# Optimization experiments

Measured on AMD Instinct MI355X. Metric: run time of the kernel, lower is better.

The kernel has to match this reference:

```python
import jax, jax.numpy as jnp
import numpy as np

N, M, FEAT, POS, D, MSG, NCLS = 64, 32, 256, 6, 262, 128, 7


def setup_inputs() -> dict:
    key = jax.random.key(0)
    ks = jax.random.split(key, 12)
    s = 0.05
    p = lambda k, shape: jax.random.normal(k, shape, jnp.float32) * s
    return {
        "nodes_feature": jax.random.normal(ks[0], (N, M, FEAT), jnp.float32),
        "pos": jax.random.normal(ks[1], (N, M, POS), jnp.float32),
        "num_rec": jax.random.randint(ks[2], (N,), 1, M + 1),
        "link_w1": p(ks[3], (D, 2 * D)),
        "link_b1": jnp.zeros((D,), jnp.float32),
        "link_w2": p(ks[4], (D,)),
        "link_b2": jnp.zeros((), jnp.float32),
        "msg_w": p(ks[5], (MSG, D)),
        "msg_b": jnp.zeros((MSG,), jnp.float32),
        "gru_w_ih": p(ks[6], (3 * D, MSG)),
        "gru_w_hh": p(ks[7], (3 * D, D)),
        "gru_b_ih": jnp.zeros((3 * D,), jnp.float32),
        "gru_b_hh": jnp.zeros((3 * D,), jnp.float32),
        "ro_w1": p(ks[8], (MSG, D)),
        "ro_b1": jnp.zeros((MSG,), jnp.float32),
        "ro_w2": p(ks[9], (NCLS, MSG)),
        "ro_b2": jnp.zeros((NCLS,), jnp.float32),
    }


def reference(nodes_feature, pos, num_rec, link_w1, link_b1, link_w2, link_b2,
              msg_w, msg_b, gru_w_ih, gru_w_hh, gru_b_ih, gru_b_hh,
              ro_w1, ro_b1, ro_w2, ro_b2):
    # node_feat = [resnet_feat, pos]  -> (N, M, 262)
    nf = jnp.concatenate([nodes_feature, pos], axis=-1)
    n, m, d = nf.shape
    valid = jnp.arange(m)[None, :] < num_rec[:, None]          # (N, M)
    pair = valid[:, :, None] & valid[:, None, :]               # (N, M, M)

    # edge_feat[b,:,i,j] = concat(nf[b,i], nf[b,j]); zero for invalid pairs
    ef = jnp.concatenate([
        jnp.broadcast_to(nf[:, :, None, :], (n, m, m, d)),
        jnp.broadcast_to(nf[:, None, :, :], (n, m, m, d)),
    ], axis=-1) * pair[..., None].astype(nf.dtype)             # (N, M, M, 2D)

    # 1x1 convs == per-pair MLP
    hlink = jax.nn.relu(jnp.einsum('bnwc,dc->bnwd', ef, link_w1) + link_b1)
    attmat = jax.nn.sigmoid(jnp.einsum('bnwd,d->bnw', hlink, link_w2) + link_b2)

    # messages are only summed over valid sender nodes w
    att_m = attmat * valid[:, None, :].astype(attmat.dtype)    # (N, M, M)

    def gru_step(x, h):
        # PyTorch GRU cell: gates order (r, z, n)
        gx = x @ gru_w_ih.T + gru_b_ih
        gh = h @ gru_w_hh.T + gru_b_hh
        xr, xz, xn = jnp.split(gx, 3, axis=-1)
        hr, hz, hn = jnp.split(gh, 3, axis=-1)
        r = jax.nn.sigmoid(xr + hr)
        z = jax.nn.sigmoid(xz + hz)
        c = jnp.tanh(xn + r * hn)
        return (1.0 - z) * c + z * h

    vmask = valid[..., None].astype(nf.dtype)
    h_state = nf                                               # pass 0 input state
    for _ in range(2):                                         # two message-passing rounds
        msg = h_state @ msg_w.T + msg_b                        # (N, M, 128)
        m_v = jnp.einsum('bnw,bwk->bnk', att_m, msg)           # attention-weighted sum
        h_state = gru_step(m_v, h_state) * vmask               # invalid nodes stay zero

    pred = (jax.nn.relu(h_state @ ro_w1.T + ro_b1) @ ro_w2.T + ro_b2) * vmask
    return pred, attmat
```

## Files before the change

### kernel.cpp

```cpp
#include <hip/hip_runtime.h>
#include <math.h>

#define N_G   64
#define M_N   32
#define FEAT  256
#define POSD  6
#define D     262
#define MSG   128
#define NCLS  7

#define KHW   288
#define KFULL 416
#define HSTR  416
#define PSTR  320

#define S_PROJ (528*288)
#define S_MSG  (128*288)
#define S_RZ   (544*416)
#define S_XN   (272*128)
#define S_HN   (272*288)
#define S_RO   (128*288)
#define S_RO2  (16*128)

#define O_WPROJ 0u
#define O_WMSG  76032u
#define O_WRZ   94464u
#define O_WXN   207616u
#define O_WHN   225024u
#define O_WRO   264192u
#define O_WRO2  282624u
#define O_GB    283648u
#define O_GHA   284736u
#define O_GHB   710720u
#define O_GPA   1136704u
#define O_GPB   1464384u
#define O_GATT  1792064u
#define O_GMSG  1833024u
#define O_B1P   1996864u
#define O_W2P   1997184u

typedef __attribute__((ext_vector_type(8))) short short8;
typedef __attribute__((ext_vector_type(4))) short short4v;
typedef __attribute__((ext_vector_type(4))) float floatx4;

#define MFMA __builtin_amdgcn_mfma_f32_16x16x32_bf16

__device__ __forceinline__ short f2bf(float f) {
    union { float f; unsigned u; } v; v.f = f;
    unsigned r = v.u + 0x7FFF + ((v.u >> 16) & 1);
    return (short)(r >> 16);
}
__device__ __forceinline__ float bf2f(short s) {
    union { float f; unsigned u; } v;
    v.u = ((unsigned)(unsigned short)s) << 16;
    return v.f;
}
__device__ __forceinline__ float sigf(float x) {
    return __builtin_amdgcn_rcpf(1.f + __expf(-x));
}
__device__ __forceinline__ float tanh_fast(float x) {
    float e = __expf(-2.f * fabsf(x));
    float t = (1.f - e) * __builtin_amdgcn_rcpf(1.f + e);
    return copysignf(t, x);
}

__global__ __launch_bounds__(256) void prep_kernel(
    const float* __restrict__ w1, const float* __restrict__ msg_w,
    const float* __restrict__ w_ih, const float* __restrict__ w_hh,
    const float* __restrict__ ro_w1, const float* __restrict__ ro_w2,
    const float* __restrict__ b_ih, const float* __restrict__ b_hh,
    const float* __restrict__ b1g, const float* __restrict__ w2g,
    const float* __restrict__ nodes, const float* __restrict__ pos,
    float* __restrict__ ws)
{
    short* wproj = (short*)(ws + O_WPROJ);
    short* wmsg  = (short*)(ws + O_WMSG);
    short* wrz   = (short*)(ws + O_WRZ);
    short* wxn   = (short*)(ws + O_WXN);
    short* whn   = (short*)(ws + O_WHN);
    short* wro   = (short*)(ws + O_WRO);
    short* wro2  = (short*)(ws + O_WRO2);
    float* gb    = ws + O_GB;

    int row = blockIdx.x * 4 + (threadIdx.x >> 6);
    const int lane = threadIdx.x & 63;
    if (row >= 5989) return;

    if (row < 528) {
        const int n = row;
        short* out = wproj + n * 288;
        const float* src = (n < D) ? (w1 + n * 524) : (w1 + (n - D) * 524 + D);
        for (int k = lane; k < 288; k += 64)
            out[k] = f2bf((k < D && n < 524) ? src[k] : 0.f);
        return;
    }
    row -= 528;
    if (row < 128) {
        short* out = wmsg + row * 288;
        const float* src = msg_w + row * D;
        for (int k = lane; k < 288; k += 64)
            out[k] = f2bf(k < D ? src[k] : 0.f);
        return;
    }
    row -= 128;
    if (row < 544) {
        const int g = row;
        const int gi = (g < 272) ? 0 : 1;
        const int d = g - gi * 272;
        short* out = wrz + g * 416;
        if (d < D) {
            const int r = gi * D + d;
            const float* sih = w_ih + r * MSG;
            const float* shh = w_hh + r * D - 128;
            for (int k = lane; k < 416; k += 64) {
                float v;
                if (k < 128)            v = sih[k];
                else if (k < 128 + D)   v = shh[k];
                else                    v = 0.f;
                out[k] = f2bf(v);
            }
        } else {
            for (int k = lane; k < 416; k += 64) out[k] = 0;
        }
        return;
    }
    row -= 544;
    if (row < 272) {
        const int d = row;
        short* out = wxn + d * 128;
        const float* src = w_ih + (2 * D + d) * MSG;
        for (int k = lane; k < 128; k += 64)
            out[k] = f2bf(d < D ? src[k] : 0.f);
        return;
    }
    row -= 272;
    if (row < 272) {
        const int d = row;
        short* out = whn + d * 288;
        const float* src = w_hh + (2 * D + d) * D;
        for (int k = lane; k < 288; k += 64)
            out[k] = f2bf((d < D && k < D) ? src[k] : 0.f);
        return;
    }
    row -= 272;
    if (row < 128) {
        short* out = wro + row * 288;
        const float* src = ro_w1 + row * D;
        for (int k = lane; k < 288; k += 64)
            out[k] = f2bf(k < D ? src[k] : 0.f);
        return;
    }
    row -= 128;
    if (row < 16) {
        short* out = wro2 + row * 128;
        const float* src = ro_w2 + row * MSG;
        for (int k = lane; k < 128; k += 64)
            out[k] = f2bf(row < NCLS ? src[k] : 0.f);
        return;
    }
    row -= 16;
    if (row < 4) {
        const int seg = row;
        float* out = gb + seg * 272;
        for (int d = lane; d < 272; d += 64) {
            float v = 0.f;
            if (d < D) {
                if (seg == 0)      v = b_ih[d] + b_hh[d];
                else if (seg == 1) v = b_ih[D + d] + b_hh[D + d];
                else if (seg == 2) v = b_ih[2 * D + d];
                else               v = b_hh[2 * D + d];
            }
            out[d] = v;
        }
        return;
    }
    row -= 4;
    if (row < 1) {
        float* b1p = ws + O_B1P;
        float* w2p = ws + O_W2P;
        for (int k = lane; k < 320; k += 64) {
            b1p[k] = (k < D) ? b1g[k] : 0.f;
            w2p[k] = (k < D) ? w2g[k] : 0.f;
        }
        return;
    }
    row -= 1;
    if (row < 2048) {
        const int b = row >> 5, w = row & 31;
        short* out = (short*)(ws + O_GHA) + (size_t)(b * 32 + w) * HSTR + 128;
        const float* nsrc = nodes + (size_t)(b * 32 + w) * FEAT;
        const float* psrc = pos + (size_t)(b * 32 + w) * POSD;
        for (int k = lane; k < 288; k += 64) {
            float v = 0.f;
            if (k < FEAT)             v = nsrc[k];
            else if (k < FEAT + POSD) v = psrc[k - FEAT];
            out[k] = f2bf(v);
        }
        return;
    }
    row -= 2048;
    {
        const int b = row >> 5, w = row & 31;
        short* hb = (short*)(ws + O_GHB) + (size_t)(b * 32 + w) * HSTR + 128;
        short* pa = (short*)(ws + O_GPA) + (size_t)(b * 32 + w) * PSTR;
        short* pb = (short*)(ws + O_GPB) + (size_t)(b * 32 + w) * PSTR;
        if (lane < 26) hb[D + lane] = 0;
        if (lane < 58) { pa[D + lane] = 0; pb[D + lane] = 0; }
    }
}

__global__ __launch_bounds__(256, 2) void k_proj(
    const float* __restrict__ ws, const float* __restrict__ msg_bg)
{
    const short* GH   = (const short*)(ws + O_GHA);
    short* GPA        = (short*)(ws + O_GPA);
    short* GPB        = (short*)(ws + O_GPB);
    short* GMSG       = (short*)(ws + O_GMSG);
    const short* Wproj = (const short*)(ws + O_WPROJ);
    const short* Wmsg  = (const short*)(ws + O_WMSG);

    const int job = blockIdx.x * 4 + (threadIdx.x >> 6);
    const int b = job / 41, t = job % 41;
    const int lane = threadIdx.x & 63;
    const int quad = lane >> 4, lrow = lane & 15;

    const short* ap0 = GH + (size_t)(b * 32 + lrow) * HSTR + 128 + quad * 8;
    const short* ap1 = ap0 + 16 * HSTR;
    const short* bw = (t < 33)
        ? Wproj + (t * 16 + lrow) * KHW + quad * 8
        : Wmsg + ((t - 33) * 16 + lrow) * KHW + quad * 8;

    short8 a0[9], a1[9], wv[9];
#pragma unroll
    for (int kk = 0; kk < 9; ++kk) {
        a0[kk] = *(const short8*)(ap0 + kk * 32);
        a1[kk] = *(const short8*)(ap1 + kk * 32);
        wv[kk] = *(const short8*)(bw + kk * 32);
    }
    floatx4 acc0 = {}, acc1 = {};
#pragma unroll
    for (int kk = 0; kk < 9; ++kk) {
        acc0 = MFMA(a0[kk], wv[kk], acc0, 0, 0, 0);
        acc1 = MFMA(a1[kk], wv[kk], acc1, 0, 0, 0);
    }
    if (t < 33) {
        int col = t * 16 + lrow;
#pragma unroll
        for (int rr = 0; rr < 4; ++rr) {
            int r0 = quad * 4 + rr;
            if (col < D) {
                GPA[(size_t)(b * 32 + r0) * PSTR + col] = f2bf(acc0[rr]);
                GPA[(size_t)(b * 32 + r0 + 16) * PSTR + col] = f2bf(acc1[rr]);
            } else if (col < 2 * D) {
                GPB[(size_t)(b * 32 + r0) * PSTR + (col - D)] = f2bf(acc0[rr]);
                GPB[(size_t)(b * 32 + r0 + 16) * PSTR + (col - D)] = f2bf(acc1[rr]);
            }
        }
    } else {
        int col = (t - 33) * 16 + lrow;
        float bias = msg_bg[col];
#pragma unroll
        for (int rr = 0; rr < 4; ++rr) {
            GMSG[(size_t)b * 5120 + col * 40 + quad * 4 + rr] = f2bf(acc0[rr] + bias);
            GMSG[(size_t)b * 5120 + col * 40 + 16 + quad * 4 + rr] = f2bf(acc1[rr] + bias);
        }
    }
}

__global__ __launch_bounds__(256, 4) void k_att(
    const float* __restrict__ ws, const int* __restrict__ nrec_g,
    const float* __restrict__ b2g, float* __restrict__ att_out)
{
    const short* GPA = (const short*)(ws + O_GPA);
    const short* GPB = (const short*)(ws + O_GPB);
    short* GATT      = (short*)(ws + O_GATT);
    const float* b1p = ws + O_B1P;
    const float* w2p = ws + O_W2P;

    const int g = blockIdx.x * 16 + (threadIdx.x >> 4);
    const int b = g >> 6;
    const int rem = g & 63;
    const int i = rem >> 1, jh = (rem & 1) * 16;
    const int c16 = threadIdx.x & 15;
    const int nr = nrec_g[b];
    const float b2v = b2g[0];

    float pav[5][4], b1v[5][4], w2v[5][4];
#pragma unroll
    for (int k = 0; k < 5; ++k) {
        int dbase = c16 * 4 + 64 * k;
        short4v p = *(const short4v*)(GPA + (size_t)(b * 32 + i) * PSTR + dbase);
        floatx4 bb = *(const floatx4*)(b1p + dbase);
        floatx4 ww = *(const floatx4*)(w2p + dbase);
#pragma unroll
        for (int e = 0; e < 4; ++e) {
            pav[k][e] = bf2f(p[e]); b1v[k][e] = bb[e]; w2v[k][e] = ww[e];
        }
    }
    float p0 = 0.f;
#pragma unroll
    for (int k = 0; k < 5; ++k)
#pragma unroll
        for (int e = 0; e < 4; ++e)
            p0 += fmaxf(b1v[k][e], 0.f) * w2v[k][e];
    p0 += __shfl_down(p0, 8, 16); p0 += __shfl_down(p0, 4, 16);
    p0 += __shfl_down(p0, 2, 16); p0 += __shfl_down(p0, 1, 16);
    float c0 = sigf(p0 + b2v);
    const bool vi = i < nr;
    for (int jj = 0; jj < 16; ++jj) {
        int j = jh + jj;
        float a;
        if (j < nr && vi) {
            const short* pb = GPB + (size_t)(b * 32 + j) * PSTR + c16 * 4;
            float s = 0.f;
#pragma unroll
            for (int k = 0; k < 5; ++k) {
                short4v q = *(const short4v*)(pb + 64 * k);
#pragma unroll
                for (int e = 0; e < 4; ++e) {
                    float v = pav[k][e] + bf2f(q[e]) + b1v[k][e];
                    s += fmaxf(v, 0.f) * w2v[k][e];
                }
            }
            s += __shfl_down(s, 8, 16); s += __shfl_down(s, 4, 16);
            s += __shfl_down(s, 2, 16); s += __shfl_down(s, 1, 16);
            a = sigf(s + b2v);
        } else {
            a = c0;
        }
        if (c16 == 0) {
            att_out[((size_t)(b * 32 + i)) * 32 + j] = a;
            GATT[(size_t)b * 1280 + i * 40 + j] = f2bf((j < nr) ? a : 0.f);
        }
    }
}

__global__ __launch_bounds__(256, 4) void k_mix0(float* __restrict__ ws)
{
    const short* GATT = (const short*)(ws + O_GATT);
    const short* GMSG = (const short*)(ws + O_GMSG);
    short* GH         = (short*)(ws + O_GHA);

    const int b = blockIdx.x;
    const int tid = threadIdx.x;
    const int ng = tid >> 6, lane = tid & 63;
    const int quad = lane >> 4, lrow = lane & 15;

    short8 af0 = *(const short8*)(GATT + (size_t)b * 1280 + lrow * 40 + quad * 8);
    short8 af1 = *(const short8*)(GATT + (size_t)b * 1280 + (16 + lrow) * 40 + quad * 8);
    short8 bf0 = *(const short8*)(GMSG + (size_t)b * 5120 + (ng * 32 + lrow) * 40 + quad * 8);
    short8 bf1 = *(const short8*)(GMSG + (size_t)b * 5120 + (ng * 32 + 16 + lrow) * 40 + quad * 8);
    floatx4 c00 = {}, c01 = {}, c10 = {}, c11 = {};
    c00 = MFMA(af0, bf0, c00, 0, 0, 0);
    c01 = MFMA(af0, bf1, c01, 0, 0, 0);
    c10 = MFMA(af1, bf0, c10, 0, 0, 0);
    c11 = MFMA(af1, bf1, c11, 0, 0, 0);
#pragma unroll
    for (int rr = 0; rr < 4; ++rr) {
        int m0 = quad * 4 + rr;
        GH[(size_t)(b * 32 + m0) * HSTR + ng * 32 + lrow] = f2bf(c00[rr]);
        GH[(size_t)(b * 32 + m0) * HSTR + ng * 32 + 16 + lrow] = f2bf(c01[rr]);
        GH[(size_t)(b * 32 + m0 + 16) * HSTR + ng * 32 + lrow] = f2bf(c10[rr]);
        GH[(size_t)(b * 32 + m0 + 16) * HSTR + ng * 32 + 16 + lrow] = f2bf(c11[rr]);
    }
}

__global__ __launch_bounds__(256, 2) void k_gru(
    float* __restrict__ ws, const int* __restrict__ nrec_g, const int srcA)
{
    const short* src = (const short*)(ws + (srcA ? O_GHA : O_GHB));
    short* dst       = (short*)(ws + (srcA ? O_GHB : O_GHA));
    const short* Wrz = (const short*)(ws + O_WRZ);
    const short* Wxn = (const short*)(ws + O_WXN);
    const short* Whn = (const short*)(ws + O_WHN);
    const float* gb  = ws + O_GB;

    const int job = blockIdx.x * 4 + (threadIdx.x >> 6);
    const int b = job / 17, s = job % 17;
    const int nr = nrec_g[b];
    const int lane = threadIdx.x & 63;
    const int quad = lane >> 4, lrow = lane & 15;

    const short* ap0 = src + (size_t)(b * 32 + lrow) * HSTR + quad * 8;
    const short* ap1 = ap0 + 16 * HSTR;
    short8 aA0[13], aA1[13];
#pragma unroll
    for (int kk = 0; kk < 13; ++kk) {
        aA0[kk] = *(const short8*)(ap0 + kk * 32);
        aA1[kk] = *(const short8*)(ap1 + kk * 32);
    }
    const short* bpr = Wrz + (s * 16 + lrow) * KFULL + quad * 8;
    const short* bpz = bpr + 272 * KFULL;
    const short* bpx = Wxn + (s * 16 + lrow) * 128 + quad * 8;
    const short* bph = Whn + (s * 16 + lrow) * KHW + quad * 8;

    short8 wr[13];
#pragma unroll
    for (int kk = 0; kk < 13; ++kk) wr[kk] = *(const short8*)(bpr + kk * 32);

    floatx4 aR0 = {}, aR1 = {}, aZ0 = {}, aZ1 = {};
    floatx4 aN0 = {}, aN1 = {}, aH0 = {}, aH1 = {};
#pragma unroll
    for (int kk = 0; kk < 13; ++kk) {
        aR0 = MFMA(aA0[kk], wr[kk], aR0, 0, 0, 0);
        aR1 = MFMA(aA1[kk], wr[kk], aR1, 0, 0, 0);
        if (kk < 4) {
            short8 bx = *(const short8*)(bpx + kk * 32);
            aN0 = MFMA(aA0[kk], bx, aN0, 0, 0, 0);
            aN1 = MFMA(aA1[kk], bx, aN1, 0, 0, 0);
        }
        wr[kk] = *(const short8*)(bpz + kk * 32);
    }
#pragma unroll
    for (int kk = 0; kk < 13; ++kk) {
        aZ0 = MFMA(aA0[kk], wr[kk], aZ0, 0, 0, 0);
        aZ1 = MFMA(aA1[kk], wr[kk], aZ1, 0, 0, 0);
        if (kk < 9) wr[kk] = *(const short8*)(bph + kk * 32);
    }
#pragma unroll
    for (int kk = 0; kk < 9; ++kk) {
        aH0 = MFMA(aA0[kk + 4], wr[kk], aH0, 0, 0, 0);
        aH1 = MFMA(aA1[kk + 4], wr[kk], aH1, 0, 0, 0);
    }

    const int d = s * 16 + lrow;
    if (d < D) {
        float bgr = gb[d], bgz = gb[272 + d];
        float bxv = gb[544 + d], bhv = gb[816 + d];
#pragma unroll
        for (int i = 0; i < 2; ++i) {
            floatx4 vR = i ? aR1 : aR0, vZ = i ? aZ1 : aZ0;
            floatx4 vN = i ? aN1 : aN0, vH = i ? aH1 : aH0;
#pragma unroll
            for (int rr = 0; rr < 4; ++rr) {
                int m = i * 16 + quad * 4 + rr;
                float rg = sigf(vR[rr] + bgr);
                float zg = sigf(vZ[rr] + bgz);
                float cg = tanh_fast(vN[rr] + bxv + rg * (vH[rr] + bhv));
                float hold = bf2f(src[(size_t)(b * 32 + m) * HSTR + 128 + d]);
                float hv = (1.f - zg) * cg + zg * hold;
                if (m >= nr) hv = 0.f;
                dst[(size_t)(b * 32 + m) * HSTR + 128 + d] = f2bf(hv);
            }
        }
    }
}

__global__ __launch_bounds__(256, 2) void k_msgmix1(
    float* __restrict__ ws, const float* __restrict__ msg_bg)
{
    __shared__ __align__(16) short msgT[128 * 40];
    short* GHB        = (short*)(ws + O_GHB);
    const short* GATT = (const short*)(ws + O_GATT);
    const short* Wmsg = (const short*)(ws + O_WMSG);

    const int b = blockIdx.x;
    const int tid = threadIdx.x;
    const int wave = tid >> 6, lane = tid & 63;
    const int quad = lane >> 4, lrow = lane & 15;

    const short* ap0 = GHB + (size_t)(b * 32 + lrow) * HSTR + 128 + quad * 8;
    const short* ap1 = ap0 + 16 * HSTR;
    short8 a0[9], a1[9];
#pragma unroll
    for (int kk = 0; kk < 9; ++kk) {
        a0[kk] = *(const short8*)(ap0 + kk * 32);
        a1[kk] = *(const short8*)(ap1 + kk * 32);
    }
#pragma unroll
    for (int ti = 0; ti < 2; ++ti) {
        int s = wave + ti * 4;
        const short* bw = Wmsg + (s * 16 + lrow) * KHW + quad * 8;
        short8 wv[9];
#pragma unroll
        for (int kk = 0; kk < 9; ++kk) wv[kk] = *(const short8*)(bw + kk * 32);
        floatx4 acc0 = {}, acc1 = {};
#pragma unroll
        for (int kk = 0; kk < 9; ++kk) {
            acc0 = MFMA(a0[kk], wv[kk], acc0, 0, 0, 0);
            acc1 = MFMA(a1[kk], wv[kk], acc1, 0, 0, 0);
        }
        int col = s * 16 + lrow;
        float bias = msg_bg[col];
#pragma unroll
        for (int rr = 0; rr < 4; ++rr) {
            msgT[col * 40 + quad * 4 + rr] = f2bf(acc0[rr] + bias);
            msgT[col * 40 + 16 + quad * 4 + rr] = f2bf(acc1[rr] + bias);
        }
    }
    __syncthreads();
    {
        const int ng = wave;
        short8 af0 = *(const short8*)(GATT + (size_t)b * 1280 + lrow * 40 + quad * 8);
        short8 af1 = *(const short8*)(GATT + (size_t)b * 1280 + (16 + lrow) * 40 + quad * 8);
        short8 bf0 = *(const short8*)(msgT + (ng * 32 + lrow) * 40 + quad * 8);
        short8 bf1 = *(const short8*)(msgT + (ng * 32 + 16 + lrow) * 40 + quad * 8);
        floatx4 c00 = {}, c01 = {}, c10 = {}, c11 = {};
        c00 = MFMA(af0, bf0, c00, 0, 0, 0);
        c01 = MFMA(af0, bf1, c01, 0, 0, 0);
        c10 = MFMA(af1, bf0, c10, 0, 0, 0);
        c11 = MFMA(af1, bf1, c11, 0, 0, 0);
#pragma unroll
        for (int rr = 0; rr < 4; ++rr) {
            int m0 = quad * 4 + rr;
            GHB[(size_t)(b * 32 + m0) * HSTR + ng * 32 + lrow] = f2bf(c00[rr]);
            GHB[(size_t)(b * 32 + m0) * HSTR + ng * 32 + 16 + lrow] = f2bf(c01[rr]);
            GHB[(size_t)(b * 32 + m0 + 16) * HSTR + ng * 32 + lrow] = f2bf(c10[rr]);
            GHB[(size_t)(b * 32 + m0 + 16) * HSTR + ng * 32 + 16 + lrow] = f2bf(c11[rr]);
        }
    }
}

__global__ __launch_bounds__(256, 2) void k_out(
    const float* __restrict__ ws, const int* __restrict__ nrec_g,
    const float* __restrict__ ro_b1g, const float* __restrict__ ro_b2g,
    float* __restrict__ pred)
{
    __shared__ __align__(16) short hidL[32 * 136];
    const short* GHA  = (const short*)(ws + O_GHA);
    const short* Wro  = (const short*)(ws + O_WRO);
    const short* Wro2 = (const short*)(ws + O_WRO2);

    const int b = blockIdx.x;
    const int tid = threadIdx.x;
    const int wave = tid >> 6, lane = tid & 63;
    const int quad = lane >> 4, lrow = lane & 15;
    const int nr = nrec_g[b];

    const short* ap0 = GHA + (size_t)(b * 32 + lrow) * HSTR + 128 + quad * 8;
    const short* ap1 = ap0 + 16 * HSTR;
    short8 a0[9], a1[9];
#pragma unroll
    for (int kk = 0; kk < 9; ++kk) {
        a0[kk] = *(const short8*)(ap0 + kk * 32);
        a1[kk] = *(const short8*)(ap1 + kk * 32);
    }
#pragma unroll
    for (int ti = 0; ti < 2; ++ti) {
        int s = wave + ti * 4;
        const short* bw = Wro + (s * 16 + lrow) * KHW + quad * 8;
        short8 wv[9];
#pragma unroll
        for (int kk = 0; kk < 9; ++kk) wv[kk] = *(const short8*)(bw + kk * 32);
        floatx4 acc0 = {}, acc1 = {};
#pragma unroll
        for (int kk = 0; kk < 9; ++kk) {
            acc0 = MFMA(a0[kk], wv[kk], acc0, 0, 0, 0);
            acc1 = MFMA(a1[kk], wv[kk], acc1, 0, 0, 0);
        }
        int col = s * 16 + lrow;
        float bias = ro_b1g[col];
#pragma unroll
        for (int rr = 0; rr < 4; ++rr) {
            hidL[(quad * 4 + rr) * 136 + col] = f2bf(fmaxf(acc0[rr] + bias, 0.f));
            hidL[(16 + quad * 4 + rr) * 136 + col] = f2bf(fmaxf(acc1[rr] + bias, 0.f));
        }
    }
    __syncthreads();
    if (wave == 0) {
        const short* bw = Wro2 + lrow * 128 + quad * 8;
        short8 wv[4];
#pragma unroll
        for (int kk = 0; kk < 4; ++kk) wv[kk] = *(const short8*)(bw + kk * 32);
        floatx4 acc0 = {}, acc1 = {};
        const short* ap = hidL + lrow * 136 + quad * 8;
#pragma unroll
        for (int kk = 0; kk < 4; ++kk) {
            short8 x0 = *(const short8*)(ap + kk * 32);
            short8 x1 = *(const short8*)(ap + 16 * 136 + kk * 32);
            acc0 = MFMA(x0, wv[kk], acc0, 0, 0, 0);
            acc1 = MFMA(x1, wv[kk], acc1, 0, 0, 0);
        }
        int q = lrow;
        if (q < NCLS) {
            float bias = ro_b2g[q];
#pragma unroll
            for (int i = 0; i < 2; ++i) {
#pragma unroll
                for (int rr = 0; rr < 4; ++rr) {
                    int m = i * 16 + quad * 4 + rr;
                    float v = (i ? acc1[rr] : acc0[rr]) + bias;
                    if (m >= nr) v = 0.f;
                    pred[((size_t)(b * 32 + m)) * NCLS + q] = v;
                }
            }
        }
    }
}

extern "C" void kernel_launch(void* const* d_in, const int* in_sizes, int n_in,
                              void* d_out, int out_size, void* d_ws, size_t ws_size,
                              hipStream_t stream)
{
    const float* nodes = (const float*)d_in[0];
    const float* pos   = (const float*)d_in[1];
    const int*   nrec  = (const int*)d_in[2];
    const float* w1    = (const float*)d_in[3];
    const float* b1    = (const float*)d_in[4];
    const float* w2    = (const float*)d_in[5];
    const float* b2    = (const float*)d_in[6];
    const float* msg_w = (const float*)d_in[7];
    const float* msg_b = (const float*)d_in[8];
    const float* w_ih  = (const float*)d_in[9];
    const float* w_hh  = (const float*)d_in[10];
    const float* b_ih  = (const float*)d_in[11];
    const float* b_hh  = (const float*)d_in[12];
    const float* ro_w1 = (const float*)d_in[13];
    const float* ro_b1 = (const float*)d_in[14];
    const float* ro_w2 = (const float*)d_in[15];
    const float* ro_b2 = (const float*)d_in[16];
    float* ws   = (float*)d_ws;
    float* pred = (float*)d_out;
    float* attout = pred + (size_t)N_G * M_N * NCLS;

    prep_kernel<<<1498, 256, 0, stream>>>(w1, msg_w, w_ih, w_hh, ro_w1, ro_w2,
                                          b_ih, b_hh, b1, w2, nodes, pos, ws);
    k_proj<<<656, 256, 0, stream>>>(ws, msg_b);
    k_att<<<256, 256, 0, stream>>>(ws, nrec, b2, attout);
    k_mix0<<<64, 256, 0, stream>>>(ws);
    k_gru<<<272, 256, 0, stream>>>(ws, nrec, 1);
    k_msgmix1<<<64, 256, 0, stream>>>(ws, msg_b);
    k_gru<<<272, 256, 0, stream>>>(ws, nrec, 0);
    k_out<<<64, 256, 0, stream>>>(ws, nrec, ro_b1, ro_b2, pred);
}
```

Baseline: 150.7 us.

## Fuse mix, GRU rounds, message and readout into one per-graph tail kernel

Replaces the five tail kernels (mix0, two GRU passes, msgmix1, readout) with a single 512-thread kernel per graph that keeps the hidden state double-buffered in shared memory across both message-passing rounds. It also prefetches the GRU weights into registers/cache at kernel start and drops the now-unneeded GHB/pad zeroing from prep. This removes several launches and global round trips of the hidden state. In exchange, only 64 blocks run the GRU, where previously it was spread over 272 blocks, so parallelism across CUs drops sharply.

```diff
diff --git a/kernel.cpp b/kernel.cpp
--- a/kernel.cpp
+++ b/kernel.cpp
@@ -9,18 +9,11 @@
 #define MSG   128
 #define NCLS  7
 
+#define KA_S  424
 #define KHW   288
 #define KFULL 416
 #define HSTR  416
 #define PSTR  320
-
-#define S_PROJ (528*288)
-#define S_MSG  (128*288)
-#define S_RZ   (544*416)
-#define S_XN   (272*128)
-#define S_HN   (272*288)
-#define S_RO   (128*288)
-#define S_RO2  (16*128)
 
 #define O_WPROJ 0u
 #define O_WMSG  76032u
@@ -31,7 +24,6 @@
 #define O_WRO2  282624u
 #define O_GB    283648u
 #define O_GHA   284736u
-#define O_GHB   710720u
 #define O_GPA   1136704u
 #define O_GPB   1464384u
 #define O_GATT  1792064u
@@ -73,22 +65,13 @@
     const float* __restrict__ nodes, const float* __restrict__ pos,
     float* __restrict__ ws)
 {
-    short* wproj = (short*)(ws + O_WPROJ);
-    short* wmsg  = (short*)(ws + O_WMSG);
-    short* wrz   = (short*)(ws + O_WRZ);
-    short* wxn   = (short*)(ws + O_WXN);
-    short* whn   = (short*)(ws + O_WHN);
-    short* wro   = (short*)(ws + O_WRO);
-    short* wro2  = (short*)(ws + O_WRO2);
-    float* gb    = ws + O_GB;
-
     int row = blockIdx.x * 4 + (threadIdx.x >> 6);
     const int lane = threadIdx.x & 63;
-    if (row >= 5989) return;
+    if (row >= 3941) return;
 
     if (row < 528) {
         const int n = row;
-        short* out = wproj + n * 288;
+        short* out = (short*)(ws + O_WPROJ) + n * 288;
         const float* src = (n < D) ? (w1 + n * 524) : (w1 + (n - D) * 524 + D);
         for (int k = lane; k < 288; k += 64)
             out[k] = f2bf((k < D && n < 524) ? src[k] : 0.f);
@@ -96,7 +79,7 @@
     }
     row -= 528;
     if (row < 128) {
-        short* out = wmsg + row * 288;
+        short* out = (short*)(ws + O_WMSG) + row * 288;
         const float* src = msg_w + row * D;
         for (int k = lane; k < 288; k += 64)
             out[k] = f2bf(k < D ? src[k] : 0.f);
@@ -107,7 +90,7 @@
         const int g = row;
         const int gi = (g < 272) ? 0 : 1;
         const int d = g - gi * 272;
-        short* out = wrz + g * 416;
+        short* out = (short*)(ws + O_WRZ) + g * 416;
         if (d < D) {
             const int r = gi * D + d;
             const float* sih = w_ih + r * MSG;
@@ -127,7 +110,7 @@
     row -= 544;
     if (row < 272) {
         const int d = row;
-        short* out = wxn + d * 128;
+        short* out = (short*)(ws + O_WXN) + d * 128;
         const float* src = w_ih + (2 * D + d) * MSG;
         for (int k = lane; k < 128; k += 64)
             out[k] = f2bf(d < D ? src[k] : 0.f);
@@ -136,7 +119,7 @@
     row -= 272;
     if (row < 272) {
         const int d = row;
-        short* out = whn + d * 288;
+        short* out = (short*)(ws + O_WHN) + d * 288;
         const float* src = w_hh + (2 * D + d) * D;
         for (int k = lane; k < 288; k += 64)
             out[k] = f2bf((d < D && k < D) ? src[k] : 0.f);
@@ -144,7 +127,7 @@
     }
     row -= 272;
     if (row < 128) {
-        short* out = wro + row * 288;
+        short* out = (short*)(ws + O_WRO) + row * 288;
         const float* src = ro_w1 + row * D;
         for (int k = lane; k < 288; k += 64)
             out[k] = f2bf(k < D ? src[k] : 0.f);
@@ -152,7 +135,7 @@
     }
     row -= 128;
     if (row < 16) {
-        short* out = wro2 + row * 128;
+        short* out = (short*)(ws + O_WRO2) + row * 128;
         const float* src = ro_w2 + row * MSG;
         for (int k = lane; k < 128; k += 64)
             out[k] = f2bf(row < NCLS ? src[k] : 0.f);
@@ -161,7 +144,7 @@
     row -= 16;
     if (row < 4) {
         const int seg = row;
-        float* out = gb + seg * 272;
+        float* out = ws + O_GB + seg * 272;
         for (int d = lane; d < 272; d += 64) {
             float v = 0.f;
             if (d < D) {
@@ -185,7 +168,7 @@
         return;
     }
     row -= 1;
-    if (row < 2048) {
+    {
         const int b = row >> 5, w = row & 31;
         short* out = (short*)(ws + O_GHA) + (size_t)(b * 32 + w) * HSTR + 128;
         const float* nsrc = nodes + (size_t)(b * 32 + w) * FEAT;
@@ -196,26 +179,16 @@
             else if (k < FEAT + POSD) v = psrc[k - FEAT];
             out[k] = f2bf(v);
         }
-        return;
-    }
-    row -= 2048;
-    {
-        const int b = row >> 5, w = row & 31;
-        short* hb = (short*)(ws + O_GHB) + (size_t)(b * 32 + w) * HSTR + 128;
-        short* pa = (short*)(ws + O_GPA) + (size_t)(b * 32 + w) * PSTR;
-        short* pb = (short*)(ws + O_GPB) + (size_t)(b * 32 + w) * PSTR;
-        if (lane < 26) hb[D + lane] = 0;
-        if (lane < 58) { pa[D + lane] = 0; pb[D + lane] = 0; }
     }
 }
 
 __global__ __launch_bounds__(256, 2) void k_proj(
     const float* __restrict__ ws, const float* __restrict__ msg_bg)
 {
-    const short* GH   = (const short*)(ws + O_GHA);
-    short* GPA        = (short*)(ws + O_GPA);
-    short* GPB        = (short*)(ws + O_GPB);
-    short* GMSG       = (short*)(ws + O_GMSG);
+    const short* GH    = (const short*)(ws + O_GHA);
+    short* GPA         = (short*)(ws + O_GPA);
+    short* GPB         = (short*)(ws + O_GPB);
+    short* GMSG        = (short*)(ws + O_GMSG);
     const short* Wproj = (const short*)(ws + O_WPROJ);
     const short* Wmsg  = (const short*)(ws + O_WMSG);
 
@@ -335,191 +308,24 @@
     }
 }
 
-__global__ __launch_bounds__(256, 4) void k_mix0(float* __restrict__ ws)
+__global__ __launch_bounds__(512, 2) void k_tail(
+    float* __restrict__ ws, const int* __restrict__ nrec_g,
+    const float* __restrict__ msg_bg, const float* __restrict__ ro_b1g,
+    const float* __restrict__ ro_b2g, float* __restrict__ pred)
 {
-    const short* GATT = (const short*)(ws + O_GATT);
-    const short* GMSG = (const short*)(ws + O_GMSG);
-    short* GH         = (short*)(ws + O_GHA);
-
-    const int b = blockIdx.x;
-    const int tid = threadIdx.x;
-    const int ng = tid >> 6, lane = tid & 63;
-    const int quad = lane >> 4, lrow = lane & 15;
-
-    short8 af0 = *(const short8*)(GATT + (size_t)b * 1280 + lrow * 40 + quad * 8);
-    short8 af1 = *(const short8*)(GATT + (size_t)b * 1280 + (16 + lrow) * 40 + quad * 8);
-    short8 bf0 = *(const short8*)(GMSG + (size_t)b * 5120 + (ng * 32 + lrow) * 40 + quad * 8);
-    short8 bf1 = *(const short8*)(GMSG + (size_t)b * 5120 + (ng * 32 + 16 + lrow) * 40 + quad * 8);
-    floatx4 c00 = {}, c01 = {}, c10 = {}, c11 = {};
-    c00 = MFMA(af0, bf0, c00, 0, 0, 0);
-    c01 = MFMA(af0, bf1, c01, 0, 0, 0);
-    c10 = MFMA(af1, bf0, c10, 0, 0, 0);
-    c11 = MFMA(af1, bf1, c11, 0, 0, 0);
-#pragma unroll
-    for (int rr = 0; rr < 4; ++rr) {
-        int m0 = quad * 4 + rr;
-        GH[(size_t)(b * 32 + m0) * HSTR + ng * 32 + lrow] = f2bf(c00[rr]);
-        GH[(size_t)(b * 32 + m0) * HSTR + ng * 32 + 16 + lrow] = f2bf(c01[rr]);
-        GH[(size_t)(b * 32 + m0 + 16) * HSTR + ng * 32 + lrow] = f2bf(c10[rr]);
-        GH[(size_t)(b * 32 + m0 + 16) * HSTR + ng * 32 + 16 + lrow] = f2bf(c11[rr]);
-    }
-}
-
-__global__ __launch_bounds__(256, 2) void k_gru(
-    float* __restrict__ ws, const int* __restrict__ nrec_g, const int srcA)
-{
-    const short* src = (const short*)(ws + (srcA ? O_GHA : O_GHB));
-    short* dst       = (short*)(ws + (srcA ? O_GHB : O_GHA));
-    const short* Wrz = (const short*)(ws + O_WRZ);
-    const short* Wxn = (const short*)(ws + O_WXN);
-    const short* Whn = (const short*)(ws + O_WHN);
-    const float* gb  = ws + O_GB;
-
-    const int job = blockIdx.x * 4 + (threadIdx.x >> 6);
-    const int b = job / 17, s = job % 17;
-    const int nr = nrec_g[b];
-    const int lane = threadIdx.x & 63;
-    const int quad = lane >> 4, lrow = lane & 15;
-
-    const short* ap0 = src + (size_t)(b * 32 + lrow) * HSTR + quad * 8;
-    const short* ap1 = ap0 + 16 * HSTR;
-    short8 aA0[13], aA1[13];
-#pragma unroll
-    for (int kk = 0; kk < 13; ++kk) {
-        aA0[kk] = *(const short8*)(ap0 + kk * 32);
-        aA1[kk] = *(const short8*)(ap1 + kk * 32);
-    }
-    const short* bpr = Wrz + (s * 16 + lrow) * KFULL + quad * 8;
-    const short* bpz = bpr + 272 * KFULL;
-    const short* bpx = Wxn + (s * 16 + lrow) * 128 + quad * 8;
-    const short* bph = Whn + (s * 16 + lrow) * KHW + quad * 8;
-
-    short8 wr[13];
-#pragma unroll
-    for (int kk = 0; kk < 13; ++kk) wr[kk] = *(const short8*)(bpr + kk * 32);
-
-    floatx4 aR0 = {}, aR1 = {}, aZ0 = {}, aZ1 = {};
-    floatx4 aN0 = {}, aN1 = {}, aH0 = {}, aH1 = {};
-#pragma unroll
-    for (int kk = 0; kk < 13; ++kk) {
-        aR0 = MFMA(aA0[kk], wr[kk], aR0, 0, 0, 0);
-        aR1 = MFMA(aA1[kk], wr[kk], aR1, 0, 0, 0);
-        if (kk < 4) {
-            short8 bx = *(const short8*)(bpx + kk * 32);
-            aN0 = MFMA(aA0[kk], bx, aN0, 0, 0, 0);
-            aN1 = MFMA(aA1[kk], bx, aN1, 0, 0, 0);
-        }
-        wr[kk] = *(const short8*)(bpz + kk * 32);
-    }
-#pragma unroll
-    for (int kk = 0; kk < 13; ++kk) {
-        aZ0 = MFMA(aA0[kk], wr[kk], aZ0, 0, 0, 0);
-        aZ1 = MFMA(aA1[kk], wr[kk], aZ1, 0, 0, 0);
-        if (kk < 9) wr[kk] = *(const short8*)(bph + kk * 32);
-    }
-#pragma unroll
-    for (int kk = 0; kk < 9; ++kk) {
-        aH0 = MFMA(aA0[kk + 4], wr[kk], aH0, 0, 0, 0);
-        aH1 = MFMA(aA1[kk + 4], wr[kk], aH1, 0, 0, 0);
-    }
-
-    const int d = s * 16 + lrow;
-    if (d < D) {
-        float bgr = gb[d], bgz = gb[272 + d];
-        float bxv = gb[544 + d], bhv = gb[816 + d];
-#pragma unroll
-        for (int i = 0; i < 2; ++i) {
-            floatx4 vR = i ? aR1 : aR0, vZ = i ? aZ1 : aZ0;
-            floatx4 vN = i ? aN1 : aN0, vH = i ? aH1 : aH0;
-#pragma unroll
-            for (int rr = 0; rr < 4; ++rr) {
-                int m = i * 16 + quad * 4 + rr;
-                float rg = sigf(vR[rr] + bgr);
-                float zg = sigf(vZ[rr] + bgz);
-                float cg = tanh_fast(vN[rr] + bxv + rg * (vH[rr] + bhv));
-                float hold = bf2f(src[(size_t)(b * 32 + m) * HSTR + 128 + d]);
-                float hv = (1.f - zg) * cg + zg * hold;
-                if (m >= nr) hv = 0.f;
-                dst[(size_t)(b * 32 + m) * HSTR + 128 + d] = f2bf(hv);
-            }
-        }
-    }
-}
-
-__global__ __launch_bounds__(256, 2) void k_msgmix1(
-    float* __restrict__ ws, const float* __restrict__ msg_bg)
-{
-    __shared__ __align__(16) short msgT[128 * 40];
-    short* GHB        = (short*)(ws + O_GHB);
-    const short* GATT = (const short*)(ws + O_GATT);
     const short* Wmsg = (const short*)(ws + O_WMSG);
-
-    const int b = blockIdx.x;
-    const int tid = threadIdx.x;
-    const int wave = tid >> 6, lane = tid & 63;
-    const int quad = lane >> 4, lrow = lane & 15;
-
-    const short* ap0 = GHB + (size_t)(b * 32 + lrow) * HSTR + 128 + quad * 8;
-    const short* ap1 = ap0 + 16 * HSTR;
-    short8 a0[9], a1[9];
-#pragma unroll
-    for (int kk = 0; kk < 9; ++kk) {
-        a0[kk] = *(const short8*)(ap0 + kk * 32);
-        a1[kk] = *(const short8*)(ap1 + kk * 32);
-    }
-#pragma unroll
-    for (int ti = 0; ti < 2; ++ti) {
-        int s = wave + ti * 4;
-        const short* bw = Wmsg + (s * 16 + lrow) * KHW + quad * 8;
-        short8 wv[9];
-#pragma unroll
-        for (int kk = 0; kk < 9; ++kk) wv[kk] = *(const short8*)(bw + kk * 32);
-        floatx4 acc0 = {}, acc1 = {};
-#pragma unroll
-        for (int kk = 0; kk < 9; ++kk) {
-            acc0 = MFMA(a0[kk], wv[kk], acc0, 0, 0, 0);
-            acc1 = MFMA(a1[kk], wv[kk], acc1, 0, 0, 0);
-        }
-        int col = s * 16 + lrow;
-        float bias = msg_bg[col];
-#pragma unroll
-        for (int rr = 0; rr < 4; ++rr) {
-            msgT[col * 40 + quad * 4 + rr] = f2bf(acc0[rr] + bias);
-            msgT[col * 40 + 16 + quad * 4 + rr] = f2bf(acc1[rr] + bias);
-        }
-    }
-    __syncthreads();
-    {
-        const int ng = wave;
-        short8 af0 = *(const short8*)(GATT + (size_t)b * 1280 + lrow * 40 + quad * 8);
-        short8 af1 = *(const short8*)(GATT + (size_t)b * 1280 + (16 + lrow) * 40 + quad * 8);
-        short8 bf0 = *(const short8*)(msgT + (ng * 32 + lrow) * 40 + quad * 8);
-        short8 bf1 = *(const short8*)(msgT + (ng * 32 + 16 + lrow) * 40 + quad * 8);
-        floatx4 c00 = {}, c01 = {}, c10 = {}, c11 = {};
-        c00 = MFMA(af0, bf0, c00, 0, 0, 0);
-        c01 = MFMA(af0, bf1, c01, 0, 0, 0);
-        c10 = MFMA(af1, bf0, c10, 0, 0, 0);
-        c11 = MFMA(af1, bf1, c11, 0, 0, 0);
-#pragma unroll
-        for (int rr = 0; rr < 4; ++rr) {
-            int m0 = quad * 4 + rr;
-            GHB[(size_t)(b * 32 + m0) * HSTR + ng * 32 + lrow] = f2bf(c00[rr]);
-            GHB[(size_t)(b * 32 + m0) * HSTR + ng * 32 + 16 + lrow] = f2bf(c01[rr]);
-            GHB[(size_t)(b * 32 + m0 + 16) * HSTR + ng * 32 + lrow] = f2bf(c10[rr]);
-            GHB[(size_t)(b * 32 + m0 + 16) * HSTR + ng * 32 + 16 + lrow] = f2bf(c11[rr]);
-        }
-    }
-}
-
-__global__ __launch_bounds__(256, 2) void k_out(
-    const float* __restrict__ ws, const int* __restrict__ nrec_g,
-    const float* __restrict__ ro_b1g, const float* __restrict__ ro_b2g,
-    float* __restrict__ pred)
-{
-    __shared__ __align__(16) short hidL[32 * 136];
-    const short* GHA  = (const short*)(ws + O_GHA);
+    const short* Wrz  = (const short*)(ws + O_WRZ);
+    const short* Wxn  = (const short*)(ws + O_WXN);
+    const short* Whn  = (const short*)(ws + O_WHN);
     const short* Wro  = (const short*)(ws + O_WRO);
     const short* Wro2 = (const short*)(ws + O_WRO2);
+    const float* gb   = ws + O_GB;
+
+    __shared__ __align__(16) short bufA[32 * KA_S];
+    __shared__ __align__(16) short bufB[32 * KA_S];
+    __shared__ __align__(16) short attL[32 * 40];
+    __shared__ __align__(16) short msgT[128 * 40];
+    __shared__ __align__(16) short hidL[32 * 136];
 
     const int b = blockIdx.x;
     const int tid = threadIdx.x;
@@ -527,26 +333,170 @@
     const int quad = lane >> 4, lrow = lane & 15;
     const int nr = nrec_g[b];
 
-    const short* ap0 = GHA + (size_t)(b * 32 + lrow) * HSTR + 128 + quad * 8;
-    const short* ap1 = ap0 + 16 * HSTR;
-    short8 a0[9], a1[9];
-#pragma unroll
-    for (int kk = 0; kk < 9; ++kk) {
-        a0[kk] = *(const short8*)(ap0 + kk * 32);
-        a1[kk] = *(const short8*)(ap1 + kk * 32);
-    }
-#pragma unroll
-    for (int ti = 0; ti < 2; ++ti) {
-        int s = wave + ti * 4;
+    floatx4 prm[10];
+    {
+        const floatx4* pb = (const floatx4*)(ws + O_WRZ);
+        const int base = wave * 64 + lane;
+#pragma unroll
+        for (int p = 0; p < 10; ++p)
+            prm[p] = pb[(p * 512 + base) * 8];
+    }
+
+    {
+        const short* GHA  = (const short*)(ws + O_GHA);
+        const short* GATT = (const short*)(ws + O_GATT);
+        const short* GMSG = (const short*)(ws + O_GMSG);
+        for (int idx = tid; idx < 32 * 36; idx += 512) {
+            int w = idx / 36, c8 = idx % 36;
+            *(short8*)(bufA + w * KA_S + 128 + c8 * 8) =
+                *(const short8*)(GHA + (size_t)(b * 32 + w) * HSTR + 128 + c8 * 8);
+        }
+        for (int idx = tid; idx < 160; idx += 512)
+            *(short8*)(attL + idx * 8) =
+                *(const short8*)(GATT + (size_t)b * 1280 + idx * 8);
+        for (int idx = tid; idx < 640; idx += 512)
+            *(short8*)(msgT + idx * 8) =
+                *(const short8*)(GMSG + (size_t)b * 5120 + idx * 8);
+        for (int idx = tid; idx < 32 * 26; idx += 512) {
+            int w = idx / 26, c = idx % 26;
+            bufB[w * KA_S + 390 + c] = 0;
+        }
+    }
+#pragma unroll
+    for (int p = 0; p < 10; ++p) asm volatile("" :: "v"(prm[p]));
+    __syncthreads();
+
+    for (int rnd = 0; rnd < 2; ++rnd) {
+        short* src = rnd ? bufB : bufA;
+        short* dst = rnd ? bufA : bufB;
+
+        if (rnd) {
+            int s = wave;
+            const short* bw = Wmsg + (s * 16 + lrow) * KHW + quad * 8;
+            short8 wm[9];
+#pragma unroll
+            for (int kk = 0; kk < 9; ++kk) wm[kk] = *(const short8*)(bw + kk * 32);
+            floatx4 acc0 = {}, acc1 = {};
+            const short* ap = src + lrow * KA_S + 128 + quad * 8;
+#pragma unroll
+            for (int kk = 0; kk < 9; ++kk) {
+                short8 x0 = *(const short8*)(ap + kk * 32);
+                short8 x1 = *(const short8*)(ap + 16 * KA_S + kk * 32);
+                acc0 = MFMA(x0, wm[kk], acc0, 0, 0, 0);
+                acc1 = MFMA(x1, wm[kk], acc1, 0, 0, 0);
+            }
+            int col = s * 16 + lrow;
+            float bias = msg_bg[col];
+#pragma unroll
+            for (int rr = 0; rr < 4; ++rr) {
+                msgT[col * 40 + quad * 4 + rr] = f2bf(acc0[rr] + bias);
+                msgT[col * 40 + 16 + quad * 4 + rr] = f2bf(acc1[rr] + bias);
+            }
+            __syncthreads();
+        }
+
+        {
+            int mi = wave & 1, ng = wave >> 1;
+            short8 afrag = *(const short8*)(attL + (mi * 16 + lrow) * 40 + quad * 8);
+            floatx4 acc0 = {}, acc1 = {};
+            short8 bf0 = *(const short8*)(msgT + (ng * 32 + lrow) * 40 + quad * 8);
+            short8 bf1 = *(const short8*)(msgT + (ng * 32 + 16 + lrow) * 40 + quad * 8);
+            acc0 = MFMA(afrag, bf0, acc0, 0, 0, 0);
+            acc1 = MFMA(afrag, bf1, acc1, 0, 0, 0);
+#pragma unroll
+            for (int rr = 0; rr < 4; ++rr) {
+                int m = mi * 16 + quad * 4 + rr;
+                src[m * KA_S + ng * 32 + lrow] = f2bf(acc0[rr]);
+                src[m * KA_S + ng * 32 + 16 + lrow] = f2bf(acc1[rr]);
+            }
+        }
+        __syncthreads();
+
+        {
+            short8 aA0[13], aA1[13];
+            {
+                const short* ap0 = src + lrow * KA_S + quad * 8;
+#pragma unroll
+                for (int kk = 0; kk < 13; ++kk) {
+                    aA0[kk] = *(const short8*)(ap0 + kk * 32);
+                    aA1[kk] = *(const short8*)(ap0 + 16 * KA_S + kk * 32);
+                }
+            }
+            for (int s = wave; s < 17; s += 8) {
+                const short* bpr = Wrz + (s * 16 + lrow) * KFULL + quad * 8;
+                const short* bpz = bpr + 272 * KFULL;
+                const short* bpx = Wxn + (s * 16 + lrow) * 128 + quad * 8;
+                const short* bph = Whn + (s * 16 + lrow) * KHW + quad * 8;
+
+                short8 wr[13];
+#pragma unroll
+                for (int kk = 0; kk < 13; ++kk) wr[kk] = *(const short8*)(bpr + kk * 32);
+
+                floatx4 aR0 = {}, aR1 = {}, aZ0 = {}, aZ1 = {};
+                floatx4 aN0 = {}, aN1 = {}, aH0 = {}, aH1 = {};
+#pragma unroll
+                for (int kk = 0; kk < 13; ++kk) {
+                    aR0 = MFMA(aA0[kk], wr[kk], aR0, 0, 0, 0);
+                    aR1 = MFMA(aA1[kk], wr[kk], aR1, 0, 0, 0);
+                    if (kk < 4) {
+                        short8 bx = *(const short8*)(bpx + kk * 32);
+                        aN0 = MFMA(aA0[kk], bx, aN0, 0, 0, 0);
+                        aN1 = MFMA(aA1[kk], bx, aN1, 0, 0, 0);
+                    }
+                    wr[kk] = *(const short8*)(bpz + kk * 32);
+                }
+#pragma unroll
+                for (int kk = 0; kk < 13; ++kk) {
+                    aZ0 = MFMA(aA0[kk], wr[kk], aZ0, 0, 0, 0);
+                    aZ1 = MFMA(aA1[kk], wr[kk], aZ1, 0, 0, 0);
+                    if (kk < 9) wr[kk] = *(const short8*)(bph + kk * 32);
+                }
+#pragma unroll
+                for (int kk = 0; kk < 9; ++kk) {
+                    aH0 = MFMA(aA0[kk + 4], wr[kk], aH0, 0, 0, 0);
+                    aH1 = MFMA(aA1[kk + 4], wr[kk], aH1, 0, 0, 0);
+                }
+
+                int d = s * 16 + lrow;
+                if (d < D) {
+                    float bgr = gb[d], bgz = gb[272 + d];
+                    float bxv = gb[544 + d], bhv = gb[816 + d];
+#pragma unroll
+                    for (int i = 0; i < 2; ++i) {
+                        floatx4 vR = i ? aR1 : aR0, vZ = i ? aZ1 : aZ0;
+                        floatx4 vN = i ? aN1 : aN0, vH = i ? aH1 : aH0;
+#pragma unroll
+                        for (int rr = 0; rr < 4; ++rr) {
+                            int m = i * 16 + quad * 4 + rr;
+                            float rg = sigf(vR[rr] + bgr);
+                            float zg = sigf(vZ[rr] + bgz);
+                            float cg = tanh_fast(vN[rr] + bxv + rg * (vH[rr] + bhv));
+                            float hold = bf2f(src[m * KA_S + 128 + d]);
+                            float hv = (1.f - zg) * cg + zg * hold;
+                            if (m >= nr) hv = 0.f;
+                            dst[m * KA_S + 128 + d] = f2bf(hv);
+                        }
+                    }
+                }
+            }
+        }
+        __syncthreads();
+    }
+
+    {
+        int s = wave;
         const short* bw = Wro + (s * 16 + lrow) * KHW + quad * 8;
         short8 wv[9];
 #pragma unroll
         for (int kk = 0; kk < 9; ++kk) wv[kk] = *(const short8*)(bw + kk * 32);
         floatx4 acc0 = {}, acc1 = {};
+        const short* ap = bufA + lrow * KA_S + 128 + quad * 8;
 #pragma unroll
         for (int kk = 0; kk < 9; ++kk) {
-            acc0 = MFMA(a0[kk], wv[kk], acc0, 0, 0, 0);
-            acc1 = MFMA(a1[kk], wv[kk], acc1, 0, 0, 0);
+            short8 x0 = *(const short8*)(ap + kk * 32);
+            short8 x1 = *(const short8*)(ap + 16 * KA_S + kk * 32);
+            acc0 = MFMA(x0, wv[kk], acc0, 0, 0, 0);
+            acc1 = MFMA(x1, wv[kk], acc1, 0, 0, 0);
         }
         int col = s * 16 + lrow;
         float bias = ro_b1g[col];
@@ -557,6 +507,7 @@
         }
     }
     __syncthreads();
+
     if (wave == 0) {
         const short* bw = Wro2 + lrow * 128 + quad * 8;
         short8 wv[4];
@@ -613,13 +564,9 @@
     float* pred = (float*)d_out;
     float* attout = pred + (size_t)N_G * M_N * NCLS;
 
-    prep_kernel<<<1498, 256, 0, stream>>>(w1, msg_w, w_ih, w_hh, ro_w1, ro_w2,
-                                          b_ih, b_hh, b1, w2, nodes, pos, ws);
+    prep_kernel<<<986, 256, 0, stream>>>(w1, msg_w, w_ih, w_hh, ro_w1, ro_w2,
+                                         b_ih, b_hh, b1, w2, nodes, pos, ws);
     k_proj<<<656, 256, 0, stream>>>(ws, msg_b);
     k_att<<<256, 256, 0, stream>>>(ws, nrec, b2, attout);
-    k_mix0<<<64, 256, 0, stream>>>(ws);
-    k_gru<<<272, 256, 0, stream>>>(ws, nrec, 1);
-    k_msgmix1<<<64, 256, 0, stream>>>(ws, msg_b);
-    k_gru<<<272, 256, 0, stream>>>(ws, nrec, 0);
-    k_out<<<64, 256, 0, stream>>>(ws, nrec, ro_b1, ro_b2, pred);
-}
+    k_tail<<<N_G, 512, 0, stream>>>(ws, nrec, msg_b, ro_b1, ro_b2, pred);
+}
```

After: 159.4 us. 5.8% more time.
